# Kernel tuning notes

Measured on AMD Instinct MI355X. Metric: run time of the kernel, lower is better.

The kernel has to match this reference:

```python
import jax, jax.numpy as jnp
import numpy as np

B, L, C = 2, 512, 64
EPS = 1e-5

def layer_norm(x, w, b):
    mu = jnp.mean(x, axis=-1, keepdims=True)
    var = jnp.mean(jnp.square(x - mu), axis=-1, keepdims=True)
    return (x - mu) * jax.lax.rsqrt(var + EPS) * w + b

def setup_inputs() -> dict:
    key = jax.random.key(0)
    ks = jax.random.split(key, 16)
    s = 1.0 / np.sqrt(C)
    def lin(k):
        k1, k2 = jax.random.split(k)
        return (jax.random.uniform(k1, (C, C), jnp.float32, -s, s),
                jax.random.uniform(k2, (C,), jnp.float32, -s, s))
    W_lp, b_lp = lin(ks[0]); W_rp, b_rp = lin(ks[1])
    W_lg, b_lg = lin(ks[2]); W_rg, b_rg = lin(ks[3])
    W_og, b_og = lin(ks[4]); W_out, b_out = lin(ks[5])
    return {
        'pairwise_states': jax.random.normal(ks[6], (B, L, L, C), jnp.float32),
        'attention_mask': jnp.ones((B, 1, 1, L), jnp.float32),
        'ln_in_w': jnp.ones((C,), jnp.float32), 'ln_in_b': jnp.zeros((C,), jnp.float32),
        'W_lp': W_lp, 'b_lp': b_lp, 'W_rp': W_rp, 'b_rp': b_rp,
        'W_lg': W_lg, 'b_lg': b_lg, 'W_rg': W_rg, 'b_rg': b_rg,
        'W_og': W_og, 'b_og': b_og,
        'ln_out_w': jnp.ones((C,), jnp.float32), 'ln_out_b': jnp.zeros((C,), jnp.float32),
        'W_out': W_out, 'b_out': b_out,
    }

def reference(pairwise_states, attention_mask, ln_in_w, ln_in_b,
              W_lp, b_lp, W_rp, b_rp, W_lg, b_lg, W_rg, b_rg,
              W_og, b_og, ln_out_w, ln_out_b, W_out, b_out):
    residual = pairwise_states
    x = layer_norm(pairwise_states, ln_in_w, ln_in_b)  # [B,L,L,C]
    left = x @ W_lp + b_lp
    right = x @ W_rp + b_rp
    # attention_mask [B,1,1,L].transpose(1,3) -> [B,L,1,1]: masks the i (row) axis
    m = jnp.transpose(attention_mask, (0, 3, 2, 1))
    left = left * m
    right = right * m
    left = left * jax.nn.sigmoid(x @ W_lg + b_lg)
    right = right * jax.nn.sigmoid(x @ W_rg + b_rg)
    out_gate = jax.nn.sigmoid(x @ W_og + b_og)
    # outgoing triangle update: out[b,i,j,c] = sum_k left[b,i,k,c] * right[b,j,k,c]
    tri = jnp.einsum('bikc,bjkc->bijc', left, right)
    y = layer_norm(tri, ln_out_w, ln_out_b) * out_gate
    y = y @ W_out + b_out
    return y + residual
```

## Files before the change

kernel.cpp:

```cpp
#include <hip/hip_runtime.h>
#include <cstdint>

typedef float f32x4 __attribute__((ext_vector_type(4)));
typedef short s16x8 __attribute__((ext_vector_type(8)));

#define APAD 72

__device__ __forceinline__ unsigned short f2bf(float f) {
  union { float f; uint32_t u; } v; v.f = f;
  uint32_t u = v.u;
  u += 0x7fffu + ((u >> 16) & 1u);
  return (unsigned short)(u >> 16);
}
__device__ __forceinline__ float bf2f(unsigned short h) {
  union { uint32_t u; float f; } v; v.u = ((uint32_t)h) << 16;
  return v.f;
}
__device__ __forceinline__ float sigmoidf_(float x) {
  return 1.0f / (1.0f + __expf(-x));
}
__device__ __forceinline__ f32x4 zero4() {
  f32x4 z = {0.f, 0.f, 0.f, 0.f};
  return z;
}
__device__ __forceinline__ void gl_lds16(const void* g, void* l) {
  __builtin_amdgcn_global_load_lds(
      (const __attribute__((address_space(1))) uint32_t*)g,
      (__attribute__((address_space(3))) uint32_t*)l, 16, 0, 0);
}

__global__ __launch_bounds__(256) void k_prep(
    const float* __restrict__ Wlp, const float* __restrict__ Wrp,
    const float* __restrict__ Wlg, const float* __restrict__ Wrg,
    const float* __restrict__ Wog, const float* __restrict__ Wout,
    unsigned short* __restrict__ wt) {
  const float* srcs[6] = {Wlp, Wrp, Wlg, Wrg, Wog, Wout};
  const int m = blockIdx.x;
  const float* W = srcs[m];
  const int t = threadIdx.x;
  for (int e = t; e < 64 * APAD; e += 256) {
    const int n = e / APAD, k = e - n * APAD;
    wt[m * (64 * APAD) + e] = (k < 64) ? f2bf(W[k * 64 + n]) : (unsigned short)0;
  }
}

__global__ __launch_bounds__(256, 4) void k1_proj(
    const float* __restrict__ xin, const float* __restrict__ mask,
    const float* __restrict__ lnw, const float* __restrict__ lnb,
    const float* __restrict__ blp, const float* __restrict__ brp,
    const float* __restrict__ blg, const float* __restrict__ brg,
    const unsigned short* __restrict__ wt,
    unsigned short* __restrict__ leftT, unsigned short* __restrict__ rightT) {
  __shared__ unsigned short A[64 * APAD];
  __shared__ unsigned short TL[64 * APAD];
  __shared__ unsigned short TR[64 * APAD];
  const int tid = threadIdx.x, lane = tid & 63, w = tid >> 6;
  const int bid = blockIdx.x;
  const int b = bid >> 12;
  const int i = (bid >> 3) & 511;
  const int k0 = (bid & 7) << 6;

  const int pair = w >> 1, ch = w & 1;
  const int kh8 = (lane >> 4) << 3;
  s16x8 wp[2][2], wg[2][2];
  float bPv[2], bGv[2];
  {
    const unsigned short* wtP = wt + (size_t)pair * (64 * APAD);
    const unsigned short* wtG = wt + (size_t)(2 + pair) * (64 * APAD);
    const float* bP = pair ? brp : blp;
    const float* bG = pair ? brg : blg;
#pragma unroll
    for (int nf2 = 0; nf2 < 2; ++nf2) {
      const int n = ch * 32 + nf2 * 16 + (lane & 15);
      const unsigned short* pp = wtP + n * APAD + kh8;
      const unsigned short* pg = wtG + n * APAD + kh8;
      wp[nf2][0] = *(const s16x8*)pp;  wp[nf2][1] = *(const s16x8*)(pp + 32);
      wg[nf2][0] = *(const s16x8*)pg;  wg[nf2][1] = *(const s16x8*)(pg + 32);
      bPv[nf2] = bP[n];  bGv[nf2] = bG[n];
    }
  }

  const int p = tid >> 2, q = tid & 3;
  const float* xrow = xin + (((size_t)b * 512 + i) * 512 + k0 + p) * 64 + q * 16;
  f32x4 xv[4];
#pragma unroll
  for (int u = 0; u < 4; ++u) xv[u] = ((const f32x4*)xrow)[u];
  float s1 = 0.f, s2 = 0.f;
#pragma unroll
  for (int u = 0; u < 4; ++u)
#pragma unroll
    for (int e = 0; e < 4; ++e) { float t = xv[u][e]; s1 += t; s2 += t * t; }
  s1 += __shfl_xor(s1, 1); s2 += __shfl_xor(s2, 1);
  s1 += __shfl_xor(s1, 2); s2 += __shfl_xor(s2, 2);
  const float mu = s1 * 0.015625f;
  const float rs = rsqrtf(s2 * 0.015625f - mu * mu + 1e-5f);
  {
    uint32_t pk[8];
#pragma unroll
    for (int u = 0; u < 4; ++u) {
      f32x4 wv = ((const f32x4*)(lnw + q * 16))[u];
      f32x4 bv = ((const f32x4*)(lnb + q * 16))[u];
#pragma unroll
      for (int e2 = 0; e2 < 2; ++e2) {
        uint32_t lo = f2bf((xv[u][2 * e2] - mu) * rs * wv[2 * e2] + bv[2 * e2]);
        uint32_t hi = f2bf((xv[u][2 * e2 + 1] - mu) * rs * wv[2 * e2 + 1] + bv[2 * e2 + 1]);
        pk[u * 2 + e2] = lo | (hi << 16);
      }
    }
    uint32_t* a32 = (uint32_t*)&A[p * APAD + q * 16];
#pragma unroll
    for (int u = 0; u < 8; ++u) a32[u] = pk[u];
  }
  const float mval = mask[b * 512 + i];
  __syncthreads();

  const int fr4 = (lane >> 4) << 2;
  unsigned short* T = pair ? TR : TL;
#pragma unroll
  for (int mf = 0; mf < 4; ++mf) {
    const int ar = (mf * 16 + (lane & 15)) * APAD + kh8;
    const s16x8 a0 = *(const s16x8*)&A[ar];
    const s16x8 a1 = *(const s16x8*)&A[ar + 32];
    f32x4 accP[2], accG[2];
#pragma unroll
    for (int nf2 = 0; nf2 < 2; ++nf2) {
      accP[nf2] = zero4(); accG[nf2] = zero4();
      accP[nf2] = __builtin_amdgcn_mfma_f32_16x16x32_bf16(a0, wp[nf2][0], accP[nf2], 0, 0, 0);
      accP[nf2] = __builtin_amdgcn_mfma_f32_16x16x32_bf16(a1, wp[nf2][1], accP[nf2], 0, 0, 0);
      accG[nf2] = __builtin_amdgcn_mfma_f32_16x16x32_bf16(a0, wg[nf2][0], accG[nf2], 0, 0, 0);
      accG[nf2] = __builtin_amdgcn_mfma_f32_16x16x32_bf16(a1, wg[nf2][1], accG[nf2], 0, 0, 0);
    }
    const int prow = mf * 16 + fr4;
#pragma unroll
    for (int nf2 = 0; nf2 < 2; ++nf2) {
      const int n = ch * 32 + nf2 * 16 + (lane & 15);
      const float bl = bPv[nf2], bg = bGv[nf2];
      float v0 = (accP[nf2][0] + bl) * mval * sigmoidf_(accG[nf2][0] + bg);
      float v1 = (accP[nf2][1] + bl) * mval * sigmoidf_(accG[nf2][1] + bg);
      float v2 = (accP[nf2][2] + bl) * mval * sigmoidf_(accG[nf2][2] + bg);
      float v3 = (accP[nf2][3] + bl) * mval * sigmoidf_(accG[nf2][3] + bg);
      *(uint32_t*)&T[n * APAD + prow] = (uint32_t)f2bf(v0) | ((uint32_t)f2bf(v1) << 16);
      *(uint32_t*)&T[n * APAD + prow + 2] = (uint32_t)f2bf(v2) | ((uint32_t)f2bf(v3) << 16);
    }
  }
  __syncthreads();

  {
    const int sn = tid >> 2, sq = tid & 3;
    const size_t gbase = (((size_t)b * 64 + sn) * 512 + i) * 512 + k0 + sq * 16;
    const uint32_t* sl = (const uint32_t*)&TL[sn * APAD + sq * 16];
    const uint32_t* sr = (const uint32_t*)&TR[sn * APAD + sq * 16];
    uint32_t* dl = (uint32_t*)(leftT + gbase);
    uint32_t* dr = (uint32_t*)(rightT + gbase);
#pragma unroll
    for (int u = 0; u < 8; ++u) dl[u] = sl[u];
#pragma unroll
    for (int u = 0; u < 8; ++u) dr[u] = sr[u];
  }
}

__global__ __launch_bounds__(256) void k2_gemm(
    const unsigned short* __restrict__ leftT,
    const unsigned short* __restrict__ rightT,
    unsigned short* __restrict__ triT) {
  __shared__ unsigned short Ab[2][128 * 64];
  __shared__ unsigned short Bb[2][128 * 64];
  const int tid = threadIdx.x, lane = tid & 63, w = tid >> 6;
  const int bid = blockIdx.x;
  const int sw = ((bid & 7) << 8) | (bid >> 3);
  const int plane = sw >> 4, tile = sw & 15;
  const size_t pb = (size_t)plane * 262144;
  const int i0 = (tile >> 2) << 7, j0 = (tile & 3) << 7;
  const int srow = lane >> 3;
  const int sk = (((lane & 7) ^ (lane >> 3)) << 3);

  f32x4 acc[4][4];
#pragma unroll
  for (int mf = 0; mf < 4; ++mf)
#pragma unroll
    for (int nf = 0; nf < 4; ++nf) acc[mf][nf] = zero4();
  const int wr = (w >> 1) << 6, wc = (w & 1) << 6;

  auto stage = [&](int buf, int kt) {
    const int kk = kt << 6;
#pragma unroll
    for (int it = 0; it < 4; ++it) {
      const int ch = it * 4 + w;
      const int row = (ch << 3) + srow;
      gl_lds16(leftT + pb + (size_t)(i0 + row) * 512 + kk + sk,
               (char*)&Ab[buf][0] + ch * 1024 + lane * 16);
      gl_lds16(rightT + pb + (size_t)(j0 + row) * 512 + kk + sk,
               (char*)&Bb[buf][0] + ch * 1024 + lane * 16);
    }
  };

  stage(0, 0);
  for (int kt = 0; kt < 8; ++kt) {
    __syncthreads();
    if (kt < 7) stage((kt & 1) ^ 1, kt + 1);
    const unsigned short* Ac = &Ab[kt & 1][0];
    const unsigned short* Bc = &Bb[kt & 1][0];
#pragma unroll
    for (int ks = 0; ks < 2; ++ks) {
      const int ko = ((lane >> 4) << 3) + (ks << 5);
      const int kosw = ko ^ ((lane & 7) << 3);
      s16x8 af[4], bfr[4];
#pragma unroll
      for (int mf = 0; mf < 4; ++mf)
        af[mf] = *(const s16x8*)&Ac[(wr + mf * 16 + (lane & 15)) * 64 + kosw];
#pragma unroll
      for (int nf = 0; nf < 4; ++nf)
        bfr[nf] = *(const s16x8*)&Bc[(wc + nf * 16 + (lane & 15)) * 64 + kosw];
#pragma unroll
      for (int mf = 0; mf < 4; ++mf)
#pragma unroll
        for (int nf = 0; nf < 4; ++nf)
          acc[mf][nf] = __builtin_amdgcn_mfma_f32_16x16x32_bf16(af[mf], bfr[nf], acc[mf][nf], 0, 0, 0);
    }
  }
  __syncthreads();
  unsigned short* Tt = &Ab[0][0];
#pragma unroll
  for (int mf = 0; mf < 4; ++mf)
#pragma unroll
    for (int nf = 0; nf < 4; ++nf) {
      const int col = wc + nf * 16 + (lane & 15);
#pragma unroll
      for (int r = 0; r < 4; ++r) {
        const int row = wr + mf * 16 + ((lane >> 4) << 2) + r;
        Tt[row * 128 + col] = f2bf(acc[mf][nf][r]);
      }
    }
  __syncthreads();
  {
    const int row = tid >> 1, half = (tid & 1) << 6;
    const uint32_t* src = (const uint32_t*)&Tt[row * 128 + half];
    uint32_t* dst = (uint32_t*)(triT + pb + (size_t)(i0 + row) * 512 + j0 + half);
#pragma unroll
    for (int u = 0; u < 32; ++u) dst[u] = src[u];
  }
}

#define OPAD 68
__global__ __launch_bounds__(256, 3) void k3_out(
    const unsigned short* __restrict__ triT,
    const float* __restrict__ resid,
    const float* __restrict__ lnw1, const float* __restrict__ lnb1,
    const float* __restrict__ bog,
    const float* __restrict__ lnw2, const float* __restrict__ lnb2,
    const float* __restrict__ bout,
    const unsigned short* __restrict__ wt,
    float* __restrict__ outp) {
  __shared__ __align__(16) unsigned char smem[18432 + 27648];
  unsigned short* WT = (unsigned short*)smem;
  unsigned short* Y  = (unsigned short*)(smem + 18432);
  unsigned short* X  = (unsigned short*)(smem + 18432 + 9216);
  unsigned short* OG = (unsigned short*)(smem + 18432 + 18432);
  float* OUT32 = (float*)(smem + 18432 + 9216);
  const int tid = threadIdx.x, lane = tid & 63, w = tid >> 6;
  const int bid = blockIdx.x;
  const int b = bid >> 12;
  const int i = (bid >> 3) & 511;
  const int j0 = (bid & 7) << 6;

  const char* wsrc = (const char*)(wt + (size_t)4 * (64 * APAD));
#pragma unroll
  for (int it = 0; it < 5; ++it) {
    const int off = (it * 256 + tid) * 16;
    if (off < 18432) gl_lds16(wsrc + off, (char*)WT + off);
  }

  const int j = tid >> 2, q = tid & 3;
  {
    const int c = tid >> 2;
    const size_t srow = ((size_t)(b * 64 + c) * 512 + i) * 512 + j0 + q * 16;
    union { uint32_t u32[8]; unsigned short s[16]; } uu;
    const uint32_t* s32 = (const uint32_t*)(triT + srow);
#pragma unroll
    for (int u = 0; u < 8; ++u) uu.u32[u] = s32[u];
#pragma unroll
    for (int s = 0; s < 16; ++s) Y[(q * 16 + s) * APAD + c] = uu.s[s];
  }
  f32x4 rv[4];
  {
    const float* rrow = resid + (((size_t)b * 512 + i) * 512 + j0 + j) * 64 + q * 16;
#pragma unroll
    for (int u = 0; u < 4; ++u) rv[u] = ((const f32x4*)rrow)[u];
    float s1 = 0.f, s2 = 0.f;
#pragma unroll
    for (int u = 0; u < 4; ++u)
#pragma unroll
      for (int e = 0; e < 4; ++e) { float t = rv[u][e]; s1 += t; s2 += t * t; }
    s1 += __shfl_xor(s1, 1); s2 += __shfl_xor(s2, 1);
    s1 += __shfl_xor(s1, 2); s2 += __shfl_xor(s2, 2);
    const float mu = s1 * 0.015625f;
    const float rs = rsqrtf(s2 * 0.015625f - mu * mu + 1e-5f);
    uint32_t pk[8];
#pragma unroll
    for (int u = 0; u < 4; ++u) {
      f32x4 wv = ((const f32x4*)(lnw1 + q * 16))[u];
      f32x4 bv = ((const f32x4*)(lnb1 + q * 16))[u];
#pragma unroll
      for (int e2 = 0; e2 < 2; ++e2) {
        uint32_t lo = f2bf((rv[u][2 * e2] - mu) * rs * wv[2 * e2] + bv[2 * e2]);
        uint32_t hi = f2bf((rv[u][2 * e2 + 1] - mu) * rs * wv[2 * e2 + 1] + bv[2 * e2 + 1]);
        pk[u * 2 + e2] = lo | (hi << 16);
      }
    }
    uint32_t* x32 = (uint32_t*)&X[j * APAD + q * 16];
#pragma unroll
    for (int u = 0; u < 8; ++u) x32[u] = pk[u];
  }
  __syncthreads();

  float yv[16];
  {
    union { uint32_t u32[8]; unsigned short s[16]; } uy;
    const uint32_t* y32 = (const uint32_t*)&Y[j * APAD + q * 16];
#pragma unroll
    for (int u = 0; u < 8; ++u) uy.u32[u] = y32[u];
#pragma unroll
    for (int s = 0; s < 16; ++s) yv[s] = bf2f(uy.s[s]);
  }
  float t1 = 0.f, t2 = 0.f;
#pragma unroll
  for (int s = 0; s < 16; ++s) { t1 += yv[s]; t2 += yv[s] * yv[s]; }
  t1 += __shfl_xor(t1, 1); t2 += __shfl_xor(t2, 1);
  t1 += __shfl_xor(t1, 2); t2 += __shfl_xor(t2, 2);
  const float mu2 = t1 * 0.015625f;
  const float rs2 = rsqrtf(t2 * 0.015625f - mu2 * mu2 + 1e-5f);

  const int arow = (w * 16 + (lane & 15)) * APAD + ((lane >> 4) << 3);
  {
    const s16x8 a0 = *(const s16x8*)&X[arow];
    const s16x8 a1 = *(const s16x8*)&X[arow + 32];
    f32x4 aog[4];
#pragma unroll
    for (int nf = 0; nf < 4; ++nf) aog[nf] = zero4();
#pragma unroll
    for (int nf = 0; nf < 4; ++nf) {
      const int brow = (nf * 16 + (lane & 15)) * APAD + ((lane >> 4) << 3);
      const s16x8 b0 = *(const s16x8*)&WT[brow];
      const s16x8 b1 = *(const s16x8*)&WT[brow + 32];
      aog[nf] = __builtin_amdgcn_mfma_f32_16x16x32_bf16(a0, b0, aog[nf], 0, 0, 0);
      aog[nf] = __builtin_amdgcn_mfma_f32_16x16x32_bf16(a1, b1, aog[nf], 0, 0, 0);
    }
#pragma unroll
    for (int nf = 0; nf < 4; ++nf) {
      const int n = nf * 16 + (lane & 15);
      const float bb = bog[n];
#pragma unroll
      for (int r = 0; r < 4; ++r) {
        const int prow = w * 16 + ((lane >> 4) << 2) + r;
        OG[prow * APAD + n] = f2bf(sigmoidf_(aog[nf][r] + bb));
      }
    }
  }
  __syncthreads();

  {
    union { uint32_t u32[8]; unsigned short s[16]; } og_;
    const uint32_t* o32 = (const uint32_t*)&OG[j * APAD + q * 16];
#pragma unroll
    for (int u = 0; u < 8; ++u) og_.u32[u] = o32[u];
    uint32_t pk[8];
#pragma unroll
    for (int u = 0; u < 4; ++u) {
      f32x4 wv = ((const f32x4*)(lnw2 + q * 16))[u];
      f32x4 bv = ((const f32x4*)(lnb2 + q * 16))[u];
#pragma unroll
      for (int e2 = 0; e2 < 2; ++e2) {
        const int s0 = u * 4 + 2 * e2;
        float y0 = ((yv[s0] - mu2) * rs2 * wv[2 * e2] + bv[2 * e2]) * bf2f(og_.s[s0]);
        float y1 = ((yv[s0 + 1] - mu2) * rs2 * wv[2 * e2 + 1] + bv[2 * e2 + 1]) * bf2f(og_.s[s0 + 1]);
        pk[u * 2 + e2] = (uint32_t)f2bf(y0) | ((uint32_t)f2bf(y1) << 16);
      }
    }
    uint32_t* y32 = (uint32_t*)&Y[j * APAD + q * 16];
#pragma unroll
    for (int u = 0; u < 8; ++u) y32[u] = pk[u];
  }
  __syncthreads();

  {
    const s16x8 a0 = *(const s16x8*)&Y[arow];
    const s16x8 a1 = *(const s16x8*)&Y[arow + 32];
    f32x4 ao[4];
#pragma unroll
    for (int nf = 0; nf < 4; ++nf) ao[nf] = zero4();
#pragma unroll
    for (int nf = 0; nf < 4; ++nf) {
      const int brow = 64 * APAD + (nf * 16 + (lane & 15)) * APAD + ((lane >> 4) << 3);
      const s16x8 b0 = *(const s16x8*)&WT[brow];
      const s16x8 b1 = *(const s16x8*)&WT[brow + 32];
      ao[nf] = __builtin_amdgcn_mfma_f32_16x16x32_bf16(a0, b0, ao[nf], 0, 0, 0);
      ao[nf] = __builtin_amdgcn_mfma_f32_16x16x32_bf16(a1, b1, ao[nf], 0, 0, 0);
    }
#pragma unroll
    for (int nf = 0; nf < 4; ++nf) {
      const int n = nf * 16 + (lane & 15);
      const float bo = bout[n];
#pragma unroll
      for (int r = 0; r < 4; ++r) {
        const int prow = w * 16 + ((lane >> 4) << 2) + r;
        OUT32[prow * OPAD + n] = ao[nf][r] + bo;
      }
    }
  }
  __syncthreads();

  {
    const size_t gb = (((size_t)b * 512 + i) * 512 + j0 + j) * 64 + q * 16;
    float* op = outp + gb;
#pragma unroll
    for (int u = 0; u < 4; ++u) {
      f32x4 ov = ((const f32x4*)&OUT32[j * OPAD + q * 16])[u];
      ((f32x4*)op)[u] = ov + rv[u];
    }
  }
}

extern "C" void kernel_launch(void* const* d_in, const int* in_sizes, int n_in,
                              void* d_out, int out_size, void* d_ws, size_t ws_size,
                              hipStream_t stream) {
  const float* x     = (const float*)d_in[0];
  const float* mask  = (const float*)d_in[1];
  const float* lnw1  = (const float*)d_in[2];
  const float* lnb1  = (const float*)d_in[3];
  const float* Wlp   = (const float*)d_in[4];
  const float* blp   = (const float*)d_in[5];
  const float* Wrp   = (const float*)d_in[6];
  const float* brp   = (const float*)d_in[7];
  const float* Wlg   = (const float*)d_in[8];
  const float* blg   = (const float*)d_in[9];
  const float* Wrg   = (const float*)d_in[10];
  const float* brg   = (const float*)d_in[11];
  const float* Wog   = (const float*)d_in[12];
  const float* bog   = (const float*)d_in[13];
  const float* lnw2  = (const float*)d_in[14];
  const float* lnb2  = (const float*)d_in[15];
  const float* Wout  = (const float*)d_in[16];
  const float* bout  = (const float*)d_in[17];

  unsigned short* leftT  = (unsigned short*)d_ws;
  unsigned short* rightT = leftT + (size_t)33554432;
  unsigned short* triT   = rightT + (size_t)33554432;
  unsigned short* wt     = triT + (size_t)33554432;

  k_prep<<<6, 256, 0, stream>>>(Wlp, Wrp, Wlg, Wrg, Wog, Wout, wt);
  k1_proj<<<8192, 256, 0, stream>>>(x, mask, lnw1, lnb1, blp, brp, blg, brg,
                                    wt, leftT, rightT);
  k2_gemm<<<2048, 256, 0, stream>>>(leftT, rightT, triT);
  k3_out<<<8192, 256, 0, stream>>>(triT, x, lnw1, lnb1, bog, lnw2, lnb2, bout,
                                   wt, (float*)d_out);
}
```

Measured before the change: 257.7 us.

## Shrink k3_out LDS footprint, swizzle Y tile, use packed bf16 converts

Cuts k3_out shared memory from 46KB to 36KB by loading the out-gate weights first and then reloading the output-projection weights into the same buffer after the gate GEMM. This lets the launch bound rise from 3 to 4 blocks per CU. It also XOR-swizzles the transposed Y tile writes and reads to reduce LDS bank conflicts, and swaps the gate MFMA operands so each lane writes packed gate values. Manual bf16 rounding is replaced by the hardware v_cvt_pk_bf16_f32 instruction in several kernels. The weight reload adds global-to-LDS traffic, and a fence may be needed before the second MFMA reads it.

```diff
diff --git a/kernel.cpp b/kernel.cpp
--- a/kernel.cpp
+++ b/kernel.cpp
@@ -15,6 +15,11 @@
 __device__ __forceinline__ float bf2f(unsigned short h) {
   union { uint32_t u; float f; } v; v.u = ((uint32_t)h) << 16;
   return v.f;
+}
+__device__ __forceinline__ uint32_t pkbf(float a, float b) {
+  uint32_t r;
+  asm("v_cvt_pk_bf16_f32 %0, %1, %2" : "=v"(r) : "v"(a), "v"(b));
+  return r;
 }
 __device__ __forceinline__ float sigmoidf_(float x) {
   return 1.0f / (1.0f + __expf(-x));
@@ -102,9 +107,8 @@
       f32x4 bv = ((const f32x4*)(lnb + q * 16))[u];
 #pragma unroll
       for (int e2 = 0; e2 < 2; ++e2) {
-        uint32_t lo = f2bf((xv[u][2 * e2] - mu) * rs * wv[2 * e2] + bv[2 * e2]);
-        uint32_t hi = f2bf((xv[u][2 * e2 + 1] - mu) * rs * wv[2 * e2 + 1] + bv[2 * e2 + 1]);
-        pk[u * 2 + e2] = lo | (hi << 16);
+        pk[u * 2 + e2] = pkbf((xv[u][2 * e2] - mu) * rs * wv[2 * e2] + bv[2 * e2],
+                              (xv[u][2 * e2 + 1] - mu) * rs * wv[2 * e2 + 1] + bv[2 * e2 + 1]);
       }
     }
     uint32_t* a32 = (uint32_t*)&A[p * APAD + q * 16];
@@ -139,8 +143,8 @@
       float v1 = (accP[nf2][1] + bl) * mval * sigmoidf_(accG[nf2][1] + bg);
       float v2 = (accP[nf2][2] + bl) * mval * sigmoidf_(accG[nf2][2] + bg);
       float v3 = (accP[nf2][3] + bl) * mval * sigmoidf_(accG[nf2][3] + bg);
-      *(uint32_t*)&T[n * APAD + prow] = (uint32_t)f2bf(v0) | ((uint32_t)f2bf(v1) << 16);
-      *(uint32_t*)&T[n * APAD + prow + 2] = (uint32_t)f2bf(v2) | ((uint32_t)f2bf(v3) << 16);
+      *(uint32_t*)&T[n * APAD + prow] = pkbf(v0, v1);
+      *(uint32_t*)&T[n * APAD + prow + 2] = pkbf(v2, v3);
     }
   }
   __syncthreads();
@@ -242,7 +246,7 @@
 }
 
 #define OPAD 68
-__global__ __launch_bounds__(256, 3) void k3_out(
+__global__ __launch_bounds__(256, 4) void k3_out(
     const unsigned short* __restrict__ triT,
     const float* __restrict__ resid,
     const float* __restrict__ lnw1, const float* __restrict__ lnb1,
@@ -251,35 +255,38 @@
     const float* __restrict__ bout,
     const unsigned short* __restrict__ wt,
     float* __restrict__ outp) {
-  __shared__ __align__(16) unsigned char smem[18432 + 27648];
+  __shared__ __align__(16) unsigned char smem[36864];
   unsigned short* WT = (unsigned short*)smem;
-  unsigned short* Y  = (unsigned short*)(smem + 18432);
-  unsigned short* X  = (unsigned short*)(smem + 18432 + 9216);
-  unsigned short* OG = (unsigned short*)(smem + 18432 + 18432);
-  float* OUT32 = (float*)(smem + 18432 + 9216);
+  unsigned short* Y  = (unsigned short*)(smem + 9216);
+  unsigned short* X  = (unsigned short*)(smem + 18432);
+  unsigned short* OG = (unsigned short*)(smem + 27648);
+  float* OUT32 = (float*)(smem + 18432);
   const int tid = threadIdx.x, lane = tid & 63, w = tid >> 6;
   const int bid = blockIdx.x;
   const int b = bid >> 12;
   const int i = (bid >> 3) & 511;
   const int j0 = (bid & 7) << 6;
 
-  const char* wsrc = (const char*)(wt + (size_t)4 * (64 * APAD));
-#pragma unroll
-  for (int it = 0; it < 5; ++it) {
-    const int off = (it * 256 + tid) * 16;
-    if (off < 18432) gl_lds16(wsrc + off, (char*)WT + off);
+  {
+    const char* wsrc = (const char*)(wt + (size_t)4 * (64 * APAD));
+#pragma unroll
+    for (int it = 0; it < 3; ++it) {
+      const int off = (it * 256 + tid) * 16;
+      if (off < 9216) gl_lds16(wsrc + off, (char*)WT + off);
+    }
   }
 
   const int j = tid >> 2, q = tid & 3;
   {
     const int c = tid >> 2;
+    const int csw = c ^ (q << 4);
     const size_t srow = ((size_t)(b * 64 + c) * 512 + i) * 512 + j0 + q * 16;
     union { uint32_t u32[8]; unsigned short s[16]; } uu;
     const uint32_t* s32 = (const uint32_t*)(triT + srow);
 #pragma unroll
     for (int u = 0; u < 8; ++u) uu.u32[u] = s32[u];
 #pragma unroll
-    for (int s = 0; s < 16; ++s) Y[(q * 16 + s) * APAD + c] = uu.s[s];
+    for (int s = 0; s < 16; ++s) Y[(q * 16 + s) * APAD + csw] = uu.s[s];
   }
   f32x4 rv[4];
   {
@@ -302,9 +309,8 @@
       f32x4 bv = ((const f32x4*)(lnb1 + q * 16))[u];
 #pragma unroll
       for (int e2 = 0; e2 < 2; ++e2) {
-        uint32_t lo = f2bf((rv[u][2 * e2] - mu) * rs * wv[2 * e2] + bv[2 * e2]);
-        uint32_t hi = f2bf((rv[u][2 * e2 + 1] - mu) * rs * wv[2 * e2 + 1] + bv[2 * e2 + 1]);
-        pk[u * 2 + e2] = lo | (hi << 16);
+        pk[u * 2 + e2] = pkbf((rv[u][2 * e2] - mu) * rs * wv[2 * e2] + bv[2 * e2],
+                              (rv[u][2 * e2 + 1] - mu) * rs * wv[2 * e2 + 1] + bv[2 * e2 + 1]);
       }
     }
     uint32_t* x32 = (uint32_t*)&X[j * APAD + q * 16];
@@ -313,10 +319,11 @@
   }
   __syncthreads();
 
+  const int qx = q ^ (w & 3);
   float yv[16];
   {
     union { uint32_t u32[8]; unsigned short s[16]; } uy;
-    const uint32_t* y32 = (const uint32_t*)&Y[j * APAD + q * 16];
+    const uint32_t* y32 = (const uint32_t*)&Y[j * APAD + (qx << 4)];
 #pragma unroll
     for (int u = 0; u < 8; ++u) uy.u32[u] = y32[u];
 #pragma unroll
@@ -330,33 +337,41 @@
   const float mu2 = t1 * 0.015625f;
   const float rs2 = rsqrtf(t2 * 0.015625f - mu2 * mu2 + 1e-5f);
 
-  const int arow = (w * 16 + (lane & 15)) * APAD + ((lane >> 4) << 3);
-  {
-    const s16x8 a0 = *(const s16x8*)&X[arow];
-    const s16x8 a1 = *(const s16x8*)&X[arow + 32];
-    f32x4 aog[4];
-#pragma unroll
-    for (int nf = 0; nf < 4; ++nf) aog[nf] = zero4();
+  const int kh8 = (lane >> 4) << 3;
+  {
+    const int xrow = (w * 16 + (lane & 15)) * APAD;
+    const s16x8 xb0 = *(const s16x8*)&X[xrow + kh8];
+    const s16x8 xb1 = *(const s16x8*)&X[xrow + kh8 + 32];
+    const int jcol = w * 16 + (lane & 15);
+    uint32_t* og32 = (uint32_t*)&OG[jcol * APAD];
 #pragma unroll
     for (int nf = 0; nf < 4; ++nf) {
-      const int brow = (nf * 16 + (lane & 15)) * APAD + ((lane >> 4) << 3);
-      const s16x8 b0 = *(const s16x8*)&WT[brow];
-      const s16x8 b1 = *(const s16x8*)&WT[brow + 32];
-      aog[nf] = __builtin_amdgcn_mfma_f32_16x16x32_bf16(a0, b0, aog[nf], 0, 0, 0);
-      aog[nf] = __builtin_amdgcn_mfma_f32_16x16x32_bf16(a1, b1, aog[nf], 0, 0, 0);
-    }
-#pragma unroll
-    for (int nf = 0; nf < 4; ++nf) {
-      const int n = nf * 16 + (lane & 15);
-      const float bb = bog[n];
-#pragma unroll
-      for (int r = 0; r < 4; ++r) {
-        const int prow = w * 16 + ((lane >> 4) << 2) + r;
-        OG[prow * APAD + n] = f2bf(sigmoidf_(aog[nf][r] + bb));
-      }
-    }
-  }
-  __syncthreads();
+      const int wrow = (nf * 16 + (lane & 15)) * APAD;
+      const s16x8 wa0 = *(const s16x8*)&WT[wrow + kh8];
+      const s16x8 wa1 = *(const s16x8*)&WT[wrow + kh8 + 32];
+      f32x4 aog = zero4();
+      aog = __builtin_amdgcn_mfma_f32_16x16x32_bf16(wa0, xb0, aog, 0, 0, 0);
+      aog = __builtin_amdgcn_mfma_f32_16x16x32_bf16(wa1, xb1, aog, 0, 0, 0);
+      const f32x4 bb4 = ((const f32x4*)bog)[(lane >> 4) + 4 * nf];
+      const float s0 = sigmoidf_(aog[0] + bb4[0]);
+      const float s1_ = sigmoidf_(aog[1] + bb4[1]);
+      const float s2_ = sigmoidf_(aog[2] + bb4[2]);
+      const float s3 = sigmoidf_(aog[3] + bb4[3]);
+      const int c2 = (lane >> 4) * 2 + nf * 8;
+      og32[c2] = pkbf(s0, s1_);
+      og32[c2 + 1] = pkbf(s2_, s3);
+    }
+  }
+  __syncthreads();
+
+  {
+    const char* wsrc2 = (const char*)(wt + (size_t)5 * (64 * APAD));
+#pragma unroll
+    for (int it = 0; it < 3; ++it) {
+      const int off = (it * 256 + tid) * 16;
+      if (off < 9216) gl_lds16(wsrc2 + off, (char*)WT + off);
+    }
+  }
 
   {
     union { uint32_t u32[8]; unsigned short s[16]; } og_;
@@ -373,24 +388,26 @@
         const int s0 = u * 4 + 2 * e2;
         float y0 = ((yv[s0] - mu2) * rs2 * wv[2 * e2] + bv[2 * e2]) * bf2f(og_.s[s0]);
         float y1 = ((yv[s0 + 1] - mu2) * rs2 * wv[2 * e2 + 1] + bv[2 * e2 + 1]) * bf2f(og_.s[s0 + 1]);
-        pk[u * 2 + e2] = (uint32_t)f2bf(y0) | ((uint32_t)f2bf(y1) << 16);
+        pk[u * 2 + e2] = pkbf(y0, y1);
       }
     }
-    uint32_t* y32 = (uint32_t*)&Y[j * APAD + q * 16];
+    uint32_t* y32 = (uint32_t*)&Y[j * APAD + (qx << 4)];
 #pragma unroll
     for (int u = 0; u < 8; ++u) y32[u] = pk[u];
   }
   __syncthreads();
 
   {
-    const s16x8 a0 = *(const s16x8*)&Y[arow];
-    const s16x8 a1 = *(const s16x8*)&Y[arow + 32];
+    const int xsw = (w & 3) << 4;
+    const int arow = (w * 16 + (lane & 15)) * APAD;
+    const s16x8 a0 = *(const s16x8*)&Y[arow + (kh8 ^ xsw)];
+    const s16x8 a1 = *(const s16x8*)&Y[arow + ((32 + kh8) ^ xsw)];
     f32x4 ao[4];
 #pragma unroll
     for (int nf = 0; nf < 4; ++nf) ao[nf] = zero4();
 #pragma unroll
     for (int nf = 0; nf < 4; ++nf) {
-      const int brow = 64 * APAD + (nf * 16 + (lane & 15)) * APAD + ((lane >> 4) << 3);
+      const int brow = (nf * 16 + (lane & 15)) * APAD + kh8;
       const s16x8 b0 = *(const s16x8*)&WT[brow];
       const s16x8 b1 = *(const s16x8*)&WT[brow + 32];
       ao[nf] = __builtin_amdgcn_mfma_f32_16x16x32_bf16(a0, b0, ao[nf], 0, 0, 0);
```

Result: faster. 249.5 us (-3.2%).
